# Performance work log

Measured on AMD Instinct MI355X. Metric: run time of the kernel, lower is better.

## Reference

```python
import jax, jax.numpy as jnp
import numpy as np

B_SZ, L, H, P = 8, 8192, 1024, 64  # batch, seq, d_inner, ssm_size
CONJ_SYM = True
DT_MIN, DT_MAX, DT_FLOOR = 1e-3, 1e-1, 1e-4


def setup_inputs() -> dict:
    key = jax.random.key(0)
    ks = jax.random.split(key, 8)
    u = jax.random.normal(ks[0], (B_SZ, L, H), dtype=jnp.float32)
    h_real = jnp.zeros((B_SZ, P), dtype=jnp.float32)
    h_imag = jnp.zeros((B_SZ, P), dtype=jnp.float32)
    # HiPPO-like stable init: Re(Lambda) = -0.5, Im(Lambda) = pi*k
    A_real = -0.5 * jnp.ones((P,), dtype=jnp.float32)
    A_imag = jnp.pi * jnp.arange(P, dtype=jnp.float32)
    local_P = 2 * P if CONJ_SYM else P
    b_scale = np.sqrt(1.0 / local_P).astype(np.float32)
    c_scale = np.sqrt(1.0 / H).astype(np.float32)
    B_real = jax.random.normal(ks[1], (P, H), dtype=jnp.float32) * b_scale
    B_imag = jax.random.normal(ks[2], (P, H), dtype=jnp.float32) * b_scale
    C_real = jax.random.normal(ks[3], (H, P), dtype=jnp.float32) * c_scale
    C_imag = jax.random.normal(ks[4], (H, P), dtype=jnp.float32) * c_scale
    D = jax.random.normal(ks[5], (H,), dtype=jnp.float32)
    # torch init: dt = exp(U(log dt_min, log dt_max)).clamp(dt_floor); inv_dt = dt + log(-expm1(-dt))
    log_dt = jax.random.uniform(ks[6], (P,), dtype=jnp.float32) \
        * (np.log(DT_MAX) - np.log(DT_MIN)) + np.log(DT_MIN)
    dt0 = jnp.clip(jnp.exp(log_dt), DT_FLOOR, None)
    inv_dt = dt0 + jnp.log(-jnp.expm1(-dt0))
    return {"u": u, "h_real": h_real, "h_imag": h_imag,
            "A_real": A_real, "A_imag": A_imag,
            "B_real": B_real, "B_imag": B_imag,
            "C_real": C_real, "C_imag": C_imag,
            "D": D, "inv_dt": inv_dt}


def reference(u, h_real, h_imag, A_real, A_imag, B_real, B_imag,
              C_real, C_imag, D, inv_dt):
    A = A_real + 1j * A_imag            # (P,)
    Bm = B_real + 1j * B_imag           # (P, H)
    Cm = C_real + 1j * C_imag           # (H, P)
    dt = jax.nn.softplus(inv_dt)        # step_rescale = 1.0
    # bilinear discretization
    den = 1.0 - (dt / 2.0) * A
    dA = (1.0 + (dt / 2.0) * A) / den   # (P,)
    dB = (dt / den)[:, None] * Bm       # (P, H)
    # input projection: Bu[b,l,p] = sum_h dB[p,h] * u[b,l,h]
    Bu = jnp.einsum('blh,ph->blp', u, dB)              # complex64 (B, L, P)
    h0 = h_real + 1j * h_imag                          # (B, P)
    Bu = Bu.at[:, 0].add(dA * h0)                      # fold initial state in
    a = jnp.broadcast_to(dA, Bu.shape)
    def combine(e1, e2):
        a1, b1 = e1
        a2, b2 = e2
        return a2 * a1, a2 * b1 + b2
    _, hs = jax.lax.associative_scan(combine, (a, Bu), axis=1)  # (B, L, P)
    yc = jnp.einsum('blp,hp->blh', hs, Cm)
    scale = 2.0 if CONJ_SYM else 1.0
    y = scale * yc.real + D * u
    h_last = hs[:, -1]
    return y, h_last.real, h_last.imag
```

## Files before the change

kernel.cpp:

```cpp
#include <hip/hip_runtime.h>

typedef unsigned short ushort_t;
typedef short s8v __attribute__((ext_vector_type(8)));
typedef unsigned short ushort8 __attribute__((ext_vector_type(8)));
typedef float floatx4 __attribute__((ext_vector_type(4)));

#define MFMA16(a, b, c) __builtin_amdgcn_mfma_f32_16x16x32_bf16((a), (b), (c), 0, 0, 0)

static constexpr int B_SZ = 8;
static constexpr int L = 8192;
static constexpr int H = 1024;
static constexpr int P = 64;
static constexpr int M_TOT = B_SZ * L;
static constexpr int S_CH = 256;
static constexpr int NC = L / S_CH;

__device__ inline ushort_t f2bf(float f) {
    union { float f; unsigned u; } v; v.f = f;
    unsigned r = v.u + 0x7fffu + ((v.u >> 16) & 1u);
    return (ushort_t)(r >> 16);
}

__global__ void params_kernel(const float* __restrict__ A_real,
                              const float* __restrict__ A_imag,
                              const float* __restrict__ inv_dt,
                              float* __restrict__ params,
                              float* __restrict__ dApow) {
    int p = threadIdx.x;
    float x = inv_dt[p];
    float dt = (x > 20.f) ? x : log1pf(expf(x));
    float ar = A_real[p], ai = A_imag[p];
    float dr = 1.f - 0.5f * dt * ar;
    float di = -0.5f * dt * ai;
    float inv = 1.f / fmaf(dr, dr, di * di);
    float nr = 1.f + 0.5f * dt * ar, ni = 0.5f * dt * ai;
    float dAr = (nr * dr + ni * di) * inv;
    float dAi = (ni * dr - nr * di) * inv;
    params[p]       = dAr;
    params[64 + p]  = dAi;
    params[128 + p] = dt * dr * inv;
    params[192 + p] = -dt * di * inv;
    float pr = 1.f, pi = 0.f;
    dApow[p] = 1.f; dApow[64 + p] = 0.f;
    for (int k = 1; k <= S_CH; k++) {
        float npr = pr * dAr - pi * dAi;
        float npi = pr * dAi + pi * dAr;
        pr = npr; pi = npi;
        dApow[k * 128 + p] = pr;
        dApow[k * 128 + 64 + p] = pi;
    }
}

__global__ void build_w(const float* __restrict__ Br, const float* __restrict__ Bi,
                        const float* __restrict__ Cr, const float* __restrict__ Ci,
                        const float* __restrict__ params,
                        ushort_t* __restrict__ W1T, ushort_t* __restrict__ CeffT) {
    int t = blockIdx.x * 256 + threadIdx.x;
    if (t < 128 * 1024) {
        int n = t >> 10, k = t & 1023;
        float v;
        if (n < 64) {
            float sr = params[128 + n], si = params[192 + n];
            v = sr * Br[n * 1024 + k] - si * Bi[n * 1024 + k];
        } else {
            int p = n - 64;
            float sr = params[128 + p], si = params[192 + p];
            v = sr * Bi[p * 1024 + k] + si * Br[p * 1024 + k];
        }
        W1T[t] = f2bf(v);
    } else {
        int t2 = t - 128 * 1024;
        int h = t2 >> 7, k = t2 & 127;
        float v = (k < 64) ? 2.f * Cr[h * 64 + k] : -2.f * Ci[h * 64 + (k - 64)];
        CeffT[t2] = f2bf(v);
    }
}

__global__ __launch_bounds__(256) void gemm1(const float* __restrict__ u,
                                             const ushort_t* __restrict__ W1T,
                                             float* __restrict__ Bu) {
    __shared__ ushort_t As[128][40];
    __shared__ ushort_t Bs[128][40];
    int tid = threadIdx.x;
    int wave = tid >> 6, lane = tid & 63;
    int q = lane >> 4, mn = lane & 15;
    size_t row0 = (size_t)blockIdx.x * 128;
    int r = tid >> 1, half = tid & 1;

    floatx4 acc[2][8] = {};

    for (int kk = 0; kk < 1024; kk += 32) {
        __syncthreads();
        {
            const float4* up = (const float4*)(u + (row0 + r) * 1024 + kk + half * 16);
            float4 f0 = up[0], f1 = up[1], f2 = up[2], f3 = up[3];
            ushort8 t0, t1;
            t0[0] = f2bf(f0.x); t0[1] = f2bf(f0.y); t0[2] = f2bf(f0.z); t0[3] = f2bf(f0.w);
            t0[4] = f2bf(f1.x); t0[5] = f2bf(f1.y); t0[6] = f2bf(f1.z); t0[7] = f2bf(f1.w);
            t1[0] = f2bf(f2.x); t1[1] = f2bf(f2.y); t1[2] = f2bf(f2.z); t1[3] = f2bf(f2.w);
            t1[4] = f2bf(f3.x); t1[5] = f2bf(f3.y); t1[6] = f2bf(f3.z); t1[7] = f2bf(f3.w);
            ushort8* dst = (ushort8*)&As[r][half * 16];
            dst[0] = t0; dst[1] = t1;
            const ushort8* wp = (const ushort8*)(W1T + r * 1024 + kk + half * 16);
            ushort8* db = (ushort8*)&Bs[r][half * 16];
            db[0] = wp[0]; db[1] = wp[1];
        }
        __syncthreads();
        s8v a0 = *(const s8v*)&As[wave * 32 + mn][q * 8];
        s8v a1 = *(const s8v*)&As[wave * 32 + 16 + mn][q * 8];
        #pragma unroll
        for (int j = 0; j < 8; j++) {
            s8v bf = *(const s8v*)&Bs[j * 16 + mn][q * 8];
            acc[0][j] = MFMA16(a0, bf, acc[0][j]);
            acc[1][j] = MFMA16(a1, bf, acc[1][j]);
        }
    }
    #pragma unroll
    for (int i = 0; i < 2; i++)
        #pragma unroll
        for (int j = 0; j < 8; j++)
            #pragma unroll
            for (int reg = 0; reg < 4; reg++) {
                size_t row = row0 + wave * 32 + i * 16 + q * 4 + reg;
                Bu[row * 128 + j * 16 + mn] = acc[i][j][reg];
            }
}

__global__ void scan_local(float* __restrict__ Bu, const float* __restrict__ params,
                           const float* __restrict__ h0r, const float* __restrict__ h0i,
                           float* __restrict__ endbuf) {
    int b = blockIdx.x >> 5;
    int c = blockIdx.x & 31;
    int p = threadIdx.x;
    float dAr = params[p], dAi = params[64 + p];
    size_t base = ((size_t)b * L + (size_t)c * S_CH) * 128 + p;
    float hr = 0.f, hi = 0.f;
    for (int l = 0; l < S_CH; l++) {
        float br = Bu[base + (size_t)l * 128];
        float bi = Bu[base + (size_t)l * 128 + 64];
        if (c == 0 && l == 0) {
            float r0 = h0r[b * 64 + p], i0 = h0i[b * 64 + p];
            br += dAr * r0 - dAi * i0;
            bi += dAr * i0 + dAi * r0;
        }
        float nhr = fmaf(dAr, hr, fmaf(-dAi, hi, br));
        float nhi = fmaf(dAr, hi, fmaf(dAi, hr, bi));
        hr = nhr; hi = nhi;
        Bu[base + (size_t)l * 128] = hr;
        Bu[base + (size_t)l * 128 + 64] = hi;
    }
    endbuf[((size_t)b * NC + c) * 128 + p] = hr;
    endbuf[((size_t)b * NC + c) * 128 + 64 + p] = hi;
}

__global__ void scan_carry(const float* __restrict__ endbuf,
                           const float* __restrict__ dApow,
                           float* __restrict__ carry) {
    int t = blockIdx.x * 64 + threadIdx.x;
    int b = t >> 6, p = t & 63;
    float aSr = dApow[S_CH * 128 + p], aSi = dApow[S_CH * 128 + 64 + p];
    float cr = 0.f, ci = 0.f;
    for (int c = 0; c < NC; c++) {
        carry[((size_t)b * NC + c) * 128 + p] = cr;
        carry[((size_t)b * NC + c) * 128 + 64 + p] = ci;
        float er = endbuf[((size_t)b * NC + c) * 128 + p];
        float ei = endbuf[((size_t)b * NC + c) * 128 + 64 + p];
        float nr = fmaf(aSr, cr, fmaf(-aSi, ci, er));
        float ni = fmaf(aSr, ci, fmaf(aSi, cr, ei));
        cr = nr; ci = ni;
    }
}

__global__ __launch_bounds__(256) void fixup(const float* __restrict__ hloc,
                                             const float* __restrict__ carry,
                                             const float* __restrict__ dApow,
                                             ushort_t* __restrict__ hfix,
                                             float* __restrict__ out_hlast) {
    size_t t = (size_t)blockIdx.x * 256 + threadIdx.x;
    size_t r = t >> 6; int p = (int)(t & 63);
    int b = (int)(r >> 13);
    int l = (int)(r & 8191);
    int c = l >> 8;
    int k = (l & (S_CH - 1)) + 1;
    float pr = dApow[k * 128 + p], pi = dApow[k * 128 + 64 + p];
    float cr = carry[((size_t)b * NC + c) * 128 + p];
    float ci = carry[((size_t)b * NC + c) * 128 + 64 + p];
    float hr = hloc[r * 128 + p] + pr * cr - pi * ci;
    float hi = hloc[r * 128 + 64 + p] + pr * ci + pi * cr;
    hfix[r * 128 + p] = f2bf(hr);
    hfix[r * 128 + 64 + p] = f2bf(hi);
    if (l == L - 1) {
        out_hlast[b * 64 + p] = hr;
        out_hlast[512 + b * 64 + p] = hi;
    }
}

__global__ __launch_bounds__(256) void gemm2(const ushort_t* __restrict__ hfix,
                                             const ushort_t* __restrict__ CeffT,
                                             const float* __restrict__ u,
                                             const float* __restrict__ D,
                                             float* __restrict__ y) {
    __shared__ ushort_t As[128][136];
    __shared__ ushort_t Bs[128][136];
    int tid = threadIdx.x;
    int wave = tid >> 6, lane = tid & 63;
    int q = lane >> 4, mn = lane & 15;
    size_t row0 = (size_t)blockIdx.x * 128;
    int r = tid >> 1, half = tid & 1;
    {
        const ushort8* src = (const ushort8*)(hfix + (row0 + r) * 128 + half * 64);
        ushort8* dst = (ushort8*)&As[r][half * 64];
        #pragma unroll
        for (int i = 0; i < 8; i++) dst[i] = src[i];
    }
    for (int ct = 0; ct < 8; ct++) {
        __syncthreads();
        {
            const ushort8* src = (const ushort8*)(CeffT + (size_t)(ct * 128 + r) * 128 + half * 64);
            ushort8* dst = (ushort8*)&Bs[r][half * 64];
            #pragma unroll
            for (int i = 0; i < 8; i++) dst[i] = src[i];
        }
        __syncthreads();
        floatx4 acc[2][8] = {};
        #pragma unroll
        for (int kk = 0; kk < 128; kk += 32) {
            s8v a0 = *(const s8v*)&As[wave * 32 + mn][kk + q * 8];
            s8v a1 = *(const s8v*)&As[wave * 32 + 16 + mn][kk + q * 8];
            #pragma unroll
            for (int j = 0; j < 8; j++) {
                s8v bf = *(const s8v*)&Bs[j * 16 + mn][kk + q * 8];
                acc[0][j] = MFMA16(a0, bf, acc[0][j]);
                acc[1][j] = MFMA16(a1, bf, acc[1][j]);
            }
        }
        float dv[8];
        #pragma unroll
        for (int j = 0; j < 8; j++) dv[j] = D[ct * 128 + j * 16 + mn];
        #pragma unroll
        for (int i = 0; i < 2; i++)
            #pragma unroll
            for (int j = 0; j < 8; j++) {
                int col = ct * 128 + j * 16 + mn;
                #pragma unroll
                for (int reg = 0; reg < 4; reg++) {
                    size_t row = row0 + wave * 32 + i * 16 + q * 4 + reg;
                    y[row * 1024 + col] = acc[i][j][reg] + dv[j] * u[row * 1024 + col];
                }
            }
    }
}

extern "C" void kernel_launch(void* const* d_in, const int* in_sizes, int n_in,
                              void* d_out, int out_size, void* d_ws, size_t ws_size,
                              hipStream_t stream) {
    const float* u      = (const float*)d_in[0];
    const float* h_r    = (const float*)d_in[1];
    const float* h_i    = (const float*)d_in[2];
    const float* A_real = (const float*)d_in[3];
    const float* A_imag = (const float*)d_in[4];
    const float* B_real = (const float*)d_in[5];
    const float* B_imag = (const float*)d_in[6];
    const float* C_real = (const float*)d_in[7];
    const float* C_imag = (const float*)d_in[8];
    const float* D      = (const float*)d_in[9];
    const float* inv_dt = (const float*)d_in[10];
    float* out = (float*)d_out;

    float* wsf       = (float*)d_ws;
    float* P_params  = wsf;
    float* P_dApow   = wsf + 1024;
    float* P_carry   = wsf + 1024 + 33024;
    float* P_end     = P_carry + 32768;
    ushort_t* P_W1T  = (ushort_t*)(P_end + 32768);
    ushort_t* P_Ceff = P_W1T + 128 * 1024;
    float* P_Bu      = (float*)(P_Ceff + 1024 * 128);
    ushort_t* P_hfix = (ushort_t*)(P_Bu + (size_t)M_TOT * 128);

    params_kernel<<<1, 64, 0, stream>>>(A_real, A_imag, inv_dt, P_params, P_dApow);
    build_w<<<1024, 256, 0, stream>>>(B_real, B_imag, C_real, C_imag, P_params, P_W1T, P_Ceff);
    gemm1<<<M_TOT / 128, 256, 0, stream>>>(u, P_W1T, P_Bu);
    scan_local<<<B_SZ * NC, 64, 0, stream>>>(P_Bu, P_params, h_r, h_i, P_end);
    scan_carry<<<8, 64, 0, stream>>>(P_end, P_dApow, P_carry);
    fixup<<<(M_TOT * 64) / 256, 256, 0, stream>>>(P_Bu, P_carry, P_dApow, P_hfix,
                                                  out + (size_t)M_TOT * H);
    gemm2<<<M_TOT / 128, 256, 0, stream>>>(P_hfix, P_Ceff, u, D, out);
}
```

Measured before the change: 624.9 us.

## Restructure scan into ends/carry/final passes with interleaved complex layout and prefetching GEMMs

```diff
diff --git a/kernel.cpp b/kernel.cpp
--- a/kernel.cpp
+++ b/kernel.cpp
@@ -10,22 +10,24 @@
 static constexpr int B_SZ = 8;
 static constexpr int L = 8192;
 static constexpr int H = 1024;
-static constexpr int P = 64;
 static constexpr int M_TOT = B_SZ * L;
-static constexpr int S_CH = 256;
+static constexpr int S_CH = 32;
 static constexpr int NC = L / S_CH;
+static constexpr int NCHUNK = B_SZ * NC;
 
 __device__ inline ushort_t f2bf(float f) {
     union { float f; unsigned u; } v; v.f = f;
     unsigned r = v.u + 0x7fffu + ((v.u >> 16) & 1u);
     return (ushort_t)(r >> 16);
 }
+__device__ inline unsigned pack_bf(float re, float im) {
+    return (unsigned)f2bf(re) | ((unsigned)f2bf(im) << 16);
+}
 
 __global__ void params_kernel(const float* __restrict__ A_real,
                               const float* __restrict__ A_imag,
                               const float* __restrict__ inv_dt,
-                              float* __restrict__ params,
-                              float* __restrict__ dApow) {
+                              float2* __restrict__ params2) {
     int p = threadIdx.x;
     float x = inv_dt[p];
     float dt = (x > 20.f) ? x : log1pf(expf(x));
@@ -36,42 +38,34 @@
     float nr = 1.f + 0.5f * dt * ar, ni = 0.5f * dt * ai;
     float dAr = (nr * dr + ni * di) * inv;
     float dAi = (ni * dr - nr * di) * inv;
-    params[p]       = dAr;
-    params[64 + p]  = dAi;
-    params[128 + p] = dt * dr * inv;
-    params[192 + p] = -dt * di * inv;
-    float pr = 1.f, pi = 0.f;
-    dApow[p] = 1.f; dApow[64 + p] = 0.f;
-    for (int k = 1; k <= S_CH; k++) {
-        float npr = pr * dAr - pi * dAi;
-        float npi = pr * dAi + pi * dAr;
-        pr = npr; pi = npi;
-        dApow[k * 128 + p] = pr;
-        dApow[k * 128 + 64 + p] = pi;
-    }
+    params2[p] = make_float2(dAr, dAi);
+    params2[64 + p] = make_float2(dt * dr * inv, -dt * di * inv);
+    float pr = dAr, pi = dAi;
+    for (int k = 1; k < S_CH; k++) {
+        float tr = pr * dAr - pi * dAi;
+        float ti = pr * dAi + pi * dAr;
+        pr = tr; pi = ti;
+    }
+    params2[128 + p] = make_float2(pr, pi);
 }
 
 __global__ void build_w(const float* __restrict__ Br, const float* __restrict__ Bi,
                         const float* __restrict__ Cr, const float* __restrict__ Ci,
-                        const float* __restrict__ params,
+                        const float2* __restrict__ params2,
                         ushort_t* __restrict__ W1T, ushort_t* __restrict__ CeffT) {
     int t = blockIdx.x * 256 + threadIdx.x;
     if (t < 128 * 1024) {
         int n = t >> 10, k = t & 1023;
-        float v;
-        if (n < 64) {
-            float sr = params[128 + n], si = params[192 + n];
-            v = sr * Br[n * 1024 + k] - si * Bi[n * 1024 + k];
-        } else {
-            int p = n - 64;
-            float sr = params[128 + p], si = params[192 + p];
-            v = sr * Bi[p * 1024 + k] + si * Br[p * 1024 + k];
-        }
+        int p = n >> 1;
+        float2 s = params2[64 + p];
+        float br = Br[p * 1024 + k], bi = Bi[p * 1024 + k];
+        float v = (n & 1) ? (s.x * bi + s.y * br) : (s.x * br - s.y * bi);
         W1T[t] = f2bf(v);
     } else {
         int t2 = t - 128 * 1024;
         int h = t2 >> 7, k = t2 & 127;
-        float v = (k < 64) ? 2.f * Cr[h * 64 + k] : -2.f * Ci[h * 64 + (k - 64)];
+        int p = k >> 1;
+        float v = (k & 1) ? -2.f * Ci[h * 64 + p] : 2.f * Cr[h * 64 + p];
         CeffT[t2] = f2bf(v);
     }
 }
@@ -79,40 +73,56 @@
 __global__ __launch_bounds__(256) void gemm1(const float* __restrict__ u,
                                              const ushort_t* __restrict__ W1T,
                                              float* __restrict__ Bu) {
-    __shared__ ushort_t As[128][40];
-    __shared__ ushort_t Bs[128][40];
+    __shared__ ushort_t As[128][72];
+    __shared__ ushort_t Bs[128][72];
     int tid = threadIdx.x;
     int wave = tid >> 6, lane = tid & 63;
     int q = lane >> 4, mn = lane & 15;
     size_t row0 = (size_t)blockIdx.x * 128;
     int r = tid >> 1, half = tid & 1;
 
+    const float* up_base = u + (row0 + r) * 1024 + half * 32;
+    const ushort_t* wp_base = W1T + r * 1024 + half * 32;
+
+    float4 fu[8];
+    ushort8 wb[4];
+    #pragma unroll
+    for (int i = 0; i < 8; i++) fu[i] = ((const float4*)up_base)[i];
+    #pragma unroll
+    for (int i = 0; i < 4; i++) wb[i] = ((const ushort8*)wp_base)[i];
+
     floatx4 acc[2][8] = {};
 
-    for (int kk = 0; kk < 1024; kk += 32) {
-        __syncthreads();
-        {
-            const float4* up = (const float4*)(u + (row0 + r) * 1024 + kk + half * 16);
-            float4 f0 = up[0], f1 = up[1], f2 = up[2], f3 = up[3];
-            ushort8 t0, t1;
-            t0[0] = f2bf(f0.x); t0[1] = f2bf(f0.y); t0[2] = f2bf(f0.z); t0[3] = f2bf(f0.w);
-            t0[4] = f2bf(f1.x); t0[5] = f2bf(f1.y); t0[6] = f2bf(f1.z); t0[7] = f2bf(f1.w);
-            t1[0] = f2bf(f2.x); t1[1] = f2bf(f2.y); t1[2] = f2bf(f2.z); t1[3] = f2bf(f2.w);
-            t1[4] = f2bf(f3.x); t1[5] = f2bf(f3.y); t1[6] = f2bf(f3.z); t1[7] = f2bf(f3.w);
-            ushort8* dst = (ushort8*)&As[r][half * 16];
-            dst[0] = t0; dst[1] = t1;
-            const ushort8* wp = (const ushort8*)(W1T + r * 1024 + kk + half * 16);
-            ushort8* db = (ushort8*)&Bs[r][half * 16];
-            db[0] = wp[0]; db[1] = wp[1];
-        }
-        __syncthreads();
-        s8v a0 = *(const s8v*)&As[wave * 32 + mn][q * 8];
-        s8v a1 = *(const s8v*)&As[wave * 32 + 16 + mn][q * 8];
-        #pragma unroll
-        for (int j = 0; j < 8; j++) {
-            s8v bf = *(const s8v*)&Bs[j * 16 + mn][q * 8];
-            acc[0][j] = MFMA16(a0, bf, acc[0][j]);
-            acc[1][j] = MFMA16(a1, bf, acc[1][j]);
+    for (int t = 0; t < 16; t++) {
+        __syncthreads();
+        #pragma unroll
+        for (int i = 0; i < 4; i++) {
+            float4 a = fu[2 * i], b = fu[2 * i + 1];
+            ushort8 v;
+            v[0] = f2bf(a.x); v[1] = f2bf(a.y); v[2] = f2bf(a.z); v[3] = f2bf(a.w);
+            v[4] = f2bf(b.x); v[5] = f2bf(b.y); v[6] = f2bf(b.z); v[7] = f2bf(b.w);
+            *(ushort8*)&As[r][half * 32 + i * 8] = v;
+            *(ushort8*)&Bs[r][half * 32 + i * 8] = wb[i];
+        }
+        __syncthreads();
+        if (t < 15) {
+            const float4* upn = (const float4*)(up_base + (t + 1) * 64);
+            #pragma unroll
+            for (int i = 0; i < 8; i++) fu[i] = upn[i];
+            const ushort8* wpn = (const ushort8*)(wp_base + (t + 1) * 64);
+            #pragma unroll
+            for (int i = 0; i < 4; i++) wb[i] = wpn[i];
+        }
+        #pragma unroll
+        for (int kk = 0; kk < 64; kk += 32) {
+            s8v a0 = *(const s8v*)&As[wave * 32 + mn][kk + q * 8];
+            s8v a1 = *(const s8v*)&As[wave * 32 + 16 + mn][kk + q * 8];
+            #pragma unroll
+            for (int j = 0; j < 8; j++) {
+                s8v bf = *(const s8v*)&Bs[j * 16 + mn][kk + q * 8];
+                acc[0][j] = MFMA16(a0, bf, acc[0][j]);
+                acc[1][j] = MFMA16(a1, bf, acc[1][j]);
+            }
         }
     }
     #pragma unroll
@@ -126,70 +136,66 @@
             }
 }
 
-__global__ void scan_local(float* __restrict__ Bu, const float* __restrict__ params,
+__global__ void scan_ends(const float2* __restrict__ Bu2,
+                          const float2* __restrict__ params2,
+                          float2* __restrict__ end2) {
+    int tid = threadIdx.x;
+    int p = tid & 63;
+    int chunk = blockIdx.x * 4 + (tid >> 6);
+    float2 dA = params2[p];
+    const float2* src = Bu2 + (size_t)chunk * (S_CH * 64) + p;
+    float hr = 0.f, hi = 0.f;
+    #pragma unroll
+    for (int l = 0; l < S_CH; l++) {
+        float2 v = src[(size_t)l * 64];
+        float nr = fmaf(dA.x, hr, fmaf(-dA.y, hi, v.x));
+        float ni = fmaf(dA.x, hi, fmaf(dA.y, hr, v.y));
+        hr = nr; hi = ni;
+    }
+    end2[(size_t)chunk * 64 + p] = make_float2(hr, hi);
+}
+
+__global__ void scan_carry(const float2* __restrict__ end2,
+                           const float2* __restrict__ params2,
                            const float* __restrict__ h0r, const float* __restrict__ h0i,
-                           float* __restrict__ endbuf) {
-    int b = blockIdx.x >> 5;
-    int c = blockIdx.x & 31;
-    int p = threadIdx.x;
-    float dAr = params[p], dAi = params[64 + p];
-    size_t base = ((size_t)b * L + (size_t)c * S_CH) * 128 + p;
-    float hr = 0.f, hi = 0.f;
+                           float2* __restrict__ carry2) {
+    int b = blockIdx.x, p = threadIdx.x;
+    float2 aS = params2[128 + p];
+    float cr = h0r[b * 64 + p], ci = h0i[b * 64 + p];
+    const float2* e = end2 + (size_t)b * NC * 64 + p;
+    float2* cw = carry2 + (size_t)b * NC * 64 + p;
+    for (int c = 0; c < NC; c++) {
+        cw[(size_t)c * 64] = make_float2(cr, ci);
+        float2 ev = e[(size_t)c * 64];
+        float nr = fmaf(aS.x, cr, fmaf(-aS.y, ci, ev.x));
+        float ni = fmaf(aS.x, ci, fmaf(aS.y, cr, ev.y));
+        cr = nr; ci = ni;
+    }
+}
+
+__global__ void scan_final(const float2* __restrict__ Bu2,
+                           const float2* __restrict__ params2,
+                           const float2* __restrict__ carry2,
+                           unsigned* __restrict__ hfix_u,
+                           float* __restrict__ out_hlast) {
+    int tid = threadIdx.x;
+    int p = tid & 63;
+    int chunk = blockIdx.x * 4 + (tid >> 6);
+    float2 dA = params2[p];
+    float2 cv = carry2[(size_t)chunk * 64 + p];
+    float hr = cv.x, hi = cv.y;
+    const float2* src = Bu2 + (size_t)chunk * (S_CH * 64) + p;
+    unsigned* dst = hfix_u + (size_t)chunk * (S_CH * 64) + p;
+    #pragma unroll
     for (int l = 0; l < S_CH; l++) {
-        float br = Bu[base + (size_t)l * 128];
-        float bi = Bu[base + (size_t)l * 128 + 64];
-        if (c == 0 && l == 0) {
-            float r0 = h0r[b * 64 + p], i0 = h0i[b * 64 + p];
-            br += dAr * r0 - dAi * i0;
-            bi += dAr * i0 + dAi * r0;
-        }
-        float nhr = fmaf(dAr, hr, fmaf(-dAi, hi, br));
-        float nhi = fmaf(dAr, hi, fmaf(dAi, hr, bi));
-        hr = nhr; hi = nhi;
-        Bu[base + (size_t)l * 128] = hr;
-        Bu[base + (size_t)l * 128 + 64] = hi;
-    }
-    endbuf[((size_t)b * NC + c) * 128 + p] = hr;
-    endbuf[((size_t)b * NC + c) * 128 + 64 + p] = hi;
-}
-
-__global__ void scan_carry(const float* __restrict__ endbuf,
-                           const float* __restrict__ dApow,
-                           float* __restrict__ carry) {
-    int t = blockIdx.x * 64 + threadIdx.x;
-    int b = t >> 6, p = t & 63;
-    float aSr = dApow[S_CH * 128 + p], aSi = dApow[S_CH * 128 + 64 + p];
-    float cr = 0.f, ci = 0.f;
-    for (int c = 0; c < NC; c++) {
-        carry[((size_t)b * NC + c) * 128 + p] = cr;
-        carry[((size_t)b * NC + c) * 128 + 64 + p] = ci;
-        float er = endbuf[((size_t)b * NC + c) * 128 + p];
-        float ei = endbuf[((size_t)b * NC + c) * 128 + 64 + p];
-        float nr = fmaf(aSr, cr, fmaf(-aSi, ci, er));
-        float ni = fmaf(aSr, ci, fmaf(aSi, cr, ei));
-        cr = nr; ci = ni;
-    }
-}
-
-__global__ __launch_bounds__(256) void fixup(const float* __restrict__ hloc,
-                                             const float* __restrict__ carry,
-                                             const float* __restrict__ dApow,
-                                             ushort_t* __restrict__ hfix,
-                                             float* __restrict__ out_hlast) {
-    size_t t = (size_t)blockIdx.x * 256 + threadIdx.x;
-    size_t r = t >> 6; int p = (int)(t & 63);
-    int b = (int)(r >> 13);
-    int l = (int)(r & 8191);
-    int c = l >> 8;
-    int k = (l & (S_CH - 1)) + 1;
-    float pr = dApow[k * 128 + p], pi = dApow[k * 128 + 64 + p];
-    float cr = carry[((size_t)b * NC + c) * 128 + p];
-    float ci = carry[((size_t)b * NC + c) * 128 + 64 + p];
-    float hr = hloc[r * 128 + p] + pr * cr - pi * ci;
-    float hi = hloc[r * 128 + 64 + p] + pr * ci + pi * cr;
-    hfix[r * 128 + p] = f2bf(hr);
-    hfix[r * 128 + 64 + p] = f2bf(hi);
-    if (l == L - 1) {
+        float2 v = src[(size_t)l * 64];
+        float nr = fmaf(dA.x, hr, fmaf(-dA.y, hi, v.x));
+        float ni = fmaf(dA.x, hi, fmaf(dA.y, hr, v.y));
+        hr = nr; hi = ni;
+        dst[(size_t)l * 64] = pack_bf(hr, hi);
+    }
+    if ((chunk & (NC - 1)) == NC - 1) {
+        int b = chunk >> 8;
         out_hlast[b * 64 + p] = hr;
         out_hlast[512 + b * 64 + p] = hi;
     }
@@ -198,7 +204,7 @@
 __global__ __launch_bounds__(256) void gemm2(const ushort_t* __restrict__ hfix,
                                              const ushort_t* __restrict__ CeffT,
                                              const float* __restrict__ u,
-                                             const float* __restrict__ D,
+                                             const float* __restrict__ Dv,
                                              float* __restrict__ y) {
     __shared__ ushort_t As[128][136];
     __shared__ ushort_t Bs[128][136];
@@ -207,21 +213,27 @@
     int q = lane >> 4, mn = lane & 15;
     size_t row0 = (size_t)blockIdx.x * 128;
     int r = tid >> 1, half = tid & 1;
+
     {
         const ushort8* src = (const ushort8*)(hfix + (row0 + r) * 128 + half * 64);
-        ushort8* dst = (ushort8*)&As[r][half * 64];
-        #pragma unroll
-        for (int i = 0; i < 8; i++) dst[i] = src[i];
-    }
+        #pragma unroll
+        for (int i = 0; i < 8; i++) *(ushort8*)&As[r][half * 64 + i * 8] = src[i];
+    }
+    const ushort_t* bbase = CeffT + (size_t)r * 128 + half * 64;
+    ushort8 breg[8];
+    #pragma unroll
+    for (int i = 0; i < 8; i++) breg[i] = ((const ushort8*)bbase)[i];
+
     for (int ct = 0; ct < 8; ct++) {
         __syncthreads();
-        {
-            const ushort8* src = (const ushort8*)(CeffT + (size_t)(ct * 128 + r) * 128 + half * 64);
-            ushort8* dst = (ushort8*)&Bs[r][half * 64];
-            #pragma unroll
-            for (int i = 0; i < 8; i++) dst[i] = src[i];
-        }
-        __syncthreads();
+        #pragma unroll
+        for (int i = 0; i < 8; i++) *(ushort8*)&Bs[r][half * 64 + i * 8] = breg[i];
+        __syncthreads();
+        if (ct < 7) {
+            const ushort8* bn = (const ushort8*)(bbase + (size_t)(ct + 1) * 128 * 128);
+            #pragma unroll
+            for (int i = 0; i < 8; i++) breg[i] = bn[i];
+        }
         floatx4 acc[2][8] = {};
         #pragma unroll
         for (int kk = 0; kk < 128; kk += 32) {
@@ -236,7 +248,7 @@
         }
         float dv[8];
         #pragma unroll
-        for (int j = 0; j < 8; j++) dv[j] = D[ct * 128 + j * 16 + mn];
+        for (int j = 0; j < 8; j++) dv[j] = Dv[ct * 128 + j * 16 + mn];
         #pragma unroll
         for (int i = 0; i < 2; i++)
             #pragma unroll
@@ -267,22 +279,20 @@
     const float* inv_dt = (const float*)d_in[10];
     float* out = (float*)d_out;
 
-    float* wsf       = (float*)d_ws;
-    float* P_params  = wsf;
-    float* P_dApow   = wsf + 1024;
-    float* P_carry   = wsf + 1024 + 33024;
-    float* P_end     = P_carry + 32768;
-    ushort_t* P_W1T  = (ushort_t*)(P_end + 32768);
+    float2* P_params = (float2*)d_ws;
+    float2* P_end    = P_params + 256;
+    float2* P_carry  = P_end + (size_t)NCHUNK * 64;
+    ushort_t* P_W1T  = (ushort_t*)(P_carry + (size_t)NCHUNK * 64);
     ushort_t* P_Ceff = P_W1T + 128 * 1024;
     float* P_Bu      = (float*)(P_Ceff + 1024 * 128);
     ushort_t* P_hfix = (ushort_t*)(P_Bu + (size_t)M_TOT * 128);
 
-    params_kernel<<<1, 64, 0, stream>>>(A_real, A_imag, inv_dt, P_params, P_dApow);
+    params_kernel<<<1, 64, 0, stream>>>(A_real, A_imag, inv_dt, P_params);
     build_w<<<1024, 256, 0, stream>>>(B_real, B_imag, C_real, C_imag, P_params, P_W1T, P_Ceff);
     gemm1<<<M_TOT / 128, 256, 0, stream>>>(u, P_W1T, P_Bu);
-    scan_local<<<B_SZ * NC, 64, 0, stream>>>(P_Bu, P_params, h_r, h_i, P_end);
-    scan_carry<<<8, 64, 0, stream>>>(P_end, P_dApow, P_carry);
-    fixup<<<(M_TOT * 64) / 256, 256, 0, stream>>>(P_Bu, P_carry, P_dApow, P_hfix,
-                                                  out + (size_t)M_TOT * H);
+    scan_ends<<<NCHUNK / 4, 256, 0, stream>>>((const float2*)P_Bu, P_params, P_end);
+    scan_carry<<<B_SZ, 64, 0, stream>>>(P_end, P_params, h_r, h_i, P_carry);
+    scan_final<<<NCHUNK / 4, 256, 0, stream>>>((const float2*)P_Bu, P_params, P_carry,
+                                               (unsigned*)P_hfix, out + (size_t)M_TOT * H);
     gemm2<<<M_TOT / 128, 256, 0, stream>>>(P_hfix, P_Ceff, u, D, out);
 }
```

After: 762.0 us. 21.9% more time.
